# Performance work log

Hardware: AMD Instinct MI355X
Metric: run time of the kernel (lower is better)

The kernel has to match this reference:

```python
import jax, jax.numpy as jnp
import numpy as np

HID = 1024

def setup_inputs() -> dict:
    key = jax.random.key(0)
    k1, k2, k3, k4, k5 = jax.random.split(key, 5)
    B, S, H = 32, 2048, HID
    hidden = jax.random.normal(k1, (B, H), dtype=jnp.float32)
    encoder_outputs = jax.random.normal(k2, (B, S, 2 * H), dtype=jnp.float32)
    # nn.Linear(3H, H): weight (H, 3H), bias (H); nn.Linear(H, 1, bias=False): weight (1, H)
    lim_a = 1.0 / np.sqrt(3 * H)
    attn_w = jax.random.uniform(k3, (H, 3 * H), minval=-lim_a, maxval=lim_a, dtype=jnp.float32)
    attn_b = jax.random.uniform(k4, (H,), minval=-lim_a, maxval=lim_a, dtype=jnp.float32)
    lim_v = 1.0 / np.sqrt(H)
    v_w = jax.random.uniform(k5, (H,), minval=-lim_v, maxval=lim_v, dtype=jnp.float32)
    return {"hidden": hidden, "encoder_outputs": encoder_outputs,
            "attn_w": attn_w, "attn_b": attn_b, "v_w": v_w}

def reference(hidden, encoder_outputs, attn_w, attn_b, v_w):
    H = hidden.shape[-1]
    # Split attn weight: columns [:H] act on the repeated hidden, [H:] on encoder_outputs.
    # Avoids materializing the (B, S, 3H) concat; math is identical.
    w_h = attn_w[:, :H]        # (H, H)
    w_e = attn_w[:, H:]        # (H, 2H)
    hid_proj = hidden @ w_h.T + attn_b            # (B, H)
    enc_proj = jnp.einsum('bse,he->bsh', encoder_outputs, w_e)  # (B, S, H)
    energy = jnp.tanh(hid_proj[:, None, :] + enc_proj)          # (B, S, H)
    scores = jnp.einsum('bsh,h->bs', energy, v_w)               # (B, S)
    attention_weights = jax.nn.softmax(scores, axis=1)          # (B, S)
    context = jnp.einsum('bs,bse->be', attention_weights, encoder_outputs)  # (B, 2H)
    return (context, attention_weights)
```

## Files before the change

### kernel.cpp

```cpp
#include <hip/hip_runtime.h>
#include <hip/hip_bf16.h>

#define AS1 __attribute__((address_space(1)))
#define AS3 __attribute__((address_space(3)))

typedef __attribute__((ext_vector_type(4))) float  f32x4;
typedef __attribute__((ext_vector_type(8))) __bf16 bf16x8;
typedef __attribute__((ext_vector_type(2))) __bf16 bf16x2;
typedef __attribute__((ext_vector_type(4))) unsigned int uint4_;

static __device__ __forceinline__ unsigned short f2bf_rne(float f) {
    unsigned int u = __builtin_bit_cast(unsigned int, f);
    u += 0x7fffu + ((u >> 16) & 1u);
    return (unsigned short)(u >> 16);
}

static __device__ __forceinline__ unsigned int pack2(float a, float b) {
#if __has_builtin(__builtin_amdgcn_cvt_pk_bf16_f32)
    bf16x2 r = __builtin_amdgcn_cvt_pk_bf16_f32(a, b);
    return __builtin_bit_cast(unsigned int, r);
#else
    return (unsigned int)f2bf_rne(a) | ((unsigned int)f2bf_rne(b) << 16);
#endif
}

__global__ __launch_bounds__(256) void convwe_kernel(
    const float* __restrict__ attn_w, unsigned short* __restrict__ Bw)
{
    const int idx = (blockIdx.x * 256 + threadIdx.x) * 8;
    const int h = idx >> 11;
    const int e = idx & 2047;
    const float* src = attn_w + h * 3072 + 1024 + e;
    f32x4 v0 = *(const f32x4*)src;
    f32x4 v1 = *(const f32x4*)(src + 4);
    uint4_ o;
    o.x = pack2(v0.x, v0.y); o.y = pack2(v0.z, v0.w);
    o.z = pack2(v1.x, v1.y); o.w = pack2(v1.z, v1.w);
    *(uint4_*)(Bw + idx) = o;
}

__global__ __launch_bounds__(256) void hidproj_kernel(
    const float* __restrict__ hidden, const float* __restrict__ attn_w,
    const float* __restrict__ attn_b, float* __restrict__ hp)
{
    __shared__ float wrow[1024];
    const int h = blockIdx.x;
    const int t = threadIdx.x;
#pragma unroll
    for (int i = 0; i < 4; ++i) wrow[t + i * 256] = attn_w[h * 3072 + t + i * 256];
    __syncthreads();
    const int wave = t >> 6, lane = t & 63;
    const float bias = attn_b[h];
    for (int b = wave; b < 32; b += 4) {
        float s = 0.f;
#pragma unroll
        for (int j = 0; j < 16; ++j)
            s = fmaf(hidden[b * 1024 + lane + j * 64], wrow[lane + j * 64], s);
#pragma unroll
        for (int off = 1; off < 64; off <<= 1) s += __shfl_xor(s, off);
        if (lane == 0) hp[b * 1024 + h] = s + bias;
    }
}

__global__ __launch_bounds__(256) void gemm_score_kernel(
    const float* __restrict__ A,
    const unsigned short* __restrict__ Bw,
    const float* __restrict__ hp,
    const float* __restrict__ vw,
    float* __restrict__ scores)
{
    __shared__ unsigned short As[128 * 32];
    __shared__ unsigned short Bs[128 * 32];

    const int id    = blockIdx.x;
    const int group = id >> 6;
    const int lid   = id & 63;
    const int mt    = group * 8 + (lid & 7);
    const int nt    = lid >> 3;
    const long tile_m = (long)mt * 128;
    const int  tile_n = nt * 128;

    const int t    = threadIdx.x;
    const int wave = t >> 6;
    const int lane = t & 63;
    const int quad = lane >> 4;
    const int l15  = lane & 15;

    const int arow = t >> 2;
    const int akc  = (t & 3) * 8;
    const float* aptr0 = A + (tile_m + arow) * 2048 + akc;
    const float* aptr1 = aptr0 + 64 * 2048;
    unsigned short* ad0 = &As[t * 8];
    unsigned short* ad1 = &As[(256 + t) * 8];

    const int bc0 = wave * 128 + lane;
    const int bc1 = bc0 + 64;
    const unsigned short* bptr0 = Bw + (tile_n + (bc0 >> 2)) * 2048 + (bc0 & 3) * 8;
    const unsigned short* bptr1 = Bw + (tile_n + (bc1 >> 2)) * 2048 + (bc1 & 3) * 8;
    unsigned short* bd0 = &Bs[(wave * 2 + 0) * 512];
    unsigned short* bd1 = &Bs[(wave * 2 + 1) * 512];

    const int wm = (wave >> 1) * 64;
    const int wn = (wave & 1) * 64;

    int aoff[4], boff[4];
#pragma unroll
    for (int i = 0; i < 4; ++i) {
        aoff[i] = (wm + i * 16 + l15) * 32 + quad * 8;
        boff[i] = (wn + i * 16 + l15) * 32 + quad * 8;
    }

    f32x4 acc[4][4];
#pragma unroll
    for (int i = 0; i < 4; ++i)
#pragma unroll
        for (int j = 0; j < 4; ++j) acc[i][j] = (f32x4){0.f, 0.f, 0.f, 0.f};

    f32x4 av0 = *(const f32x4*)aptr0;
    f32x4 av1 = *(const f32x4*)(aptr0 + 4);
    f32x4 av2 = *(const f32x4*)aptr1;
    f32x4 av3 = *(const f32x4*)(aptr1 + 4);

    for (int kt = 0; kt < 64; ++kt) {
        __syncthreads();
        __builtin_amdgcn_global_load_lds((const AS1 void*)bptr0, (AS3 void*)bd0, 16, 0, 0);
        __builtin_amdgcn_global_load_lds((const AS1 void*)bptr1, (AS3 void*)bd1, 16, 0, 0);
        bptr0 += 32; bptr1 += 32;

        uint4_ w0, w1;
        w0.x = pack2(av0.x, av0.y); w0.y = pack2(av0.z, av0.w);
        w0.z = pack2(av1.x, av1.y); w0.w = pack2(av1.z, av1.w);
        w1.x = pack2(av2.x, av2.y); w1.y = pack2(av2.z, av2.w);
        w1.z = pack2(av3.x, av3.y); w1.w = pack2(av3.z, av3.w);
        *(uint4_*)ad0 = w0;
        *(uint4_*)ad1 = w1;

        if (kt < 63) {
            aptr0 += 32; aptr1 += 32;
            av0 = *(const f32x4*)aptr0;
            av1 = *(const f32x4*)(aptr0 + 4);
            av2 = *(const f32x4*)aptr1;
            av3 = *(const f32x4*)(aptr1 + 4);
        }
        __syncthreads();

        bf16x8 af[4], bfr[4];
#pragma unroll
        for (int i = 0; i < 4; ++i) af[i]  = *(const bf16x8*)(&As[aoff[i]]);
#pragma unroll
        for (int i = 0; i < 4; ++i) bfr[i] = *(const bf16x8*)(&Bs[boff[i]]);
#pragma unroll
        for (int mi = 0; mi < 4; ++mi)
#pragma unroll
            for (int ni = 0; ni < 4; ++ni)
                acc[mi][ni] = __builtin_amdgcn_mfma_f32_16x16x32_bf16(
                    af[mi], bfr[ni], acc[mi][ni], 0, 0, 0);
    }

    const int bidx = mt >> 4;
    float vwv[4], hpv[4];
#pragma unroll
    for (int ni = 0; ni < 4; ++ni) {
        const int n = tile_n + wn + ni * 16 + l15;
        vwv[ni] = vw[n];
        hpv[ni] = hp[bidx * 1024 + n];
    }
#pragma unroll
    for (int mi = 0; mi < 4; ++mi) {
#pragma unroll
        for (int r = 0; r < 4; ++r) {
            float s = 0.f;
#pragma unroll
            for (int ni = 0; ni < 4; ++ni) {
                float x = hpv[ni] + acc[mi][ni][r];
                x = fminf(fmaxf(x, -12.f), 12.f);
                const float e  = __expf(x + x);
                const float th = (e - 1.f) * __builtin_amdgcn_rcpf(e + 1.f);
                s = fmaf(vwv[ni], th, s);
            }
            s += __shfl_xor(s, 1);
            s += __shfl_xor(s, 2);
            s += __shfl_xor(s, 4);
            s += __shfl_xor(s, 8);
            if (l15 == 0)
                atomicAdd(&scores[tile_m + wm + mi * 16 + quad * 4 + r], s);
        }
    }
}

__global__ __launch_bounds__(256) void softmax_kernel(float* __restrict__ sc)
{
    __shared__ float red[8];
    const int b = blockIdx.x, t = threadIdx.x;
    const int wave = t >> 6, lane = t & 63;
    float* p = sc + b * 2048;
    float v[8];
#pragma unroll
    for (int i = 0; i < 8; ++i) v[i] = p[t + i * 256];
    float m = v[0];
#pragma unroll
    for (int i = 1; i < 8; ++i) m = fmaxf(m, v[i]);
#pragma unroll
    for (int off = 1; off < 64; off <<= 1) m = fmaxf(m, __shfl_xor(m, off));
    if (lane == 0) red[wave] = m;
    __syncthreads();
    m = fmaxf(fmaxf(red[0], red[1]), fmaxf(red[2], red[3]));
    float s = 0.f;
#pragma unroll
    for (int i = 0; i < 8; ++i) { v[i] = __expf(v[i] - m); s += v[i]; }
#pragma unroll
    for (int off = 1; off < 64; off <<= 1) s += __shfl_xor(s, off);
    if (lane == 0) red[4 + wave] = s;
    __syncthreads();
    s = red[4] + red[5] + red[6] + red[7];
    const float inv = 1.0f / s;
#pragma unroll
    for (int i = 0; i < 8; ++i) p[t + i * 256] = v[i] * inv;
}

__global__ __launch_bounds__(256) void context_kernel(
    const float* __restrict__ enc, const float* __restrict__ attn,
    float* __restrict__ ctx)
{
    const int b  = blockIdx.x >> 5;
    const int sc = blockIdx.x & 31;
    const int t  = threadIdx.x;
    const float* ep = enc + ((long)(b * 2048 + sc * 64)) * 2048 + t * 8;
    const float* ap = attn + b * 2048 + sc * 64;
    f32x4 a0 = (f32x4){0.f, 0.f, 0.f, 0.f};
    f32x4 a1 = (f32x4){0.f, 0.f, 0.f, 0.f};
#pragma unroll 4
    for (int s = 0; s < 64; ++s) {
        const float w = ap[s];
        f32x4 v0 = *(const f32x4*)ep;
        f32x4 v1 = *(const f32x4*)(ep + 4);
        a0 += w * v0;
        a1 += w * v1;
        ep += 2048;
    }
    float* cp = ctx + b * 2048 + t * 8;
    atomicAdd(&cp[0], a0.x); atomicAdd(&cp[1], a0.y);
    atomicAdd(&cp[2], a0.z); atomicAdd(&cp[3], a0.w);
    atomicAdd(&cp[4], a1.x); atomicAdd(&cp[5], a1.y);
    atomicAdd(&cp[6], a1.z); atomicAdd(&cp[7], a1.w);
}

extern "C" void kernel_launch(void* const* d_in, const int* in_sizes, int n_in,
                              void* d_out, int out_size, void* d_ws, size_t ws_size,
                              hipStream_t stream)
{
    const float* hidden = (const float*)d_in[0];
    const float* enc    = (const float*)d_in[1];
    const float* attn_w = (const float*)d_in[2];
    const float* attn_b = (const float*)d_in[3];
    const float* vw     = (const float*)d_in[4];
    float* out = (float*)d_out;

    unsigned short* Bw = (unsigned short*)d_ws;
    float* hp = (float*)((char*)d_ws + (size_t)1024 * 2048 * 2);

    float* ctx  = out;
    float* attn = out + 65536;

    hipMemsetAsync(d_out, 0, (size_t)out_size * 4, stream);
    convwe_kernel <<<1024, 256, 0, stream>>>(attn_w, Bw);
    hidproj_kernel<<<1024, 256, 0, stream>>>(hidden, attn_w, attn_b, hp);
    gemm_score_kernel<<<4096, 256, 0, stream>>>(enc, Bw, hp, vw, attn);
    softmax_kernel<<<32, 256, 0, stream>>>(attn);
    context_kernel<<<1024, 256, 0, stream>>>(enc, attn, ctx);
}
```

Measured before the change: 1.205 ms.

## Pre-convert encoder outputs to bf16 and split context into partial sums plus reduce

Adds a pass that converts the full encoder_outputs tensor to bf16 in workspace. The GEMM can then load both A and B tiles with direct global-to-LDS loads, so the per-iteration fp32 load and pack of A goes away. The context reduction also changes from per-element global atomics to per-chunk partial sums followed by a reduce kernel. Both paths are chosen only when the workspace is large enough. The conversion adds a 512MB read and a 256MB write, which may cost more than the GEMM saves.

```diff
diff --git a/kernel.cpp b/kernel.cpp
--- a/kernel.cpp
+++ b/kernel.cpp
@@ -39,6 +39,18 @@
     *(uint4_*)(Bw + idx) = o;
 }
 
+__global__ __launch_bounds__(256) void convenc_kernel(
+    const float* __restrict__ enc, unsigned short* __restrict__ dst)
+{
+    const size_t idx = ((size_t)blockIdx.x * 256 + threadIdx.x) * 8;
+    f32x4 v0 = *(const f32x4*)(enc + idx);
+    f32x4 v1 = *(const f32x4*)(enc + idx + 4);
+    uint4_ o;
+    o.x = pack2(v0.x, v0.y); o.y = pack2(v0.z, v0.w);
+    o.z = pack2(v1.x, v1.y); o.w = pack2(v1.z, v1.w);
+    *(uint4_*)(dst + idx) = o;
+}
+
 __global__ __launch_bounds__(256) void hidproj_kernel(
     const float* __restrict__ hidden, const float* __restrict__ attn_w,
     const float* __restrict__ attn_b, float* __restrict__ hp)
@@ -62,8 +74,8 @@
     }
 }
 
-__global__ __launch_bounds__(256) void gemm_score_kernel(
-    const float* __restrict__ A,
+__global__ __launch_bounds__(256) void gemm_score_bf16_kernel(
+    const unsigned short* __restrict__ Abf,
     const unsigned short* __restrict__ Bw,
     const float* __restrict__ hp,
     const float* __restrict__ vw,
@@ -86,19 +98,16 @@
     const int quad = lane >> 4;
     const int l15  = lane & 15;
 
-    const int arow = t >> 2;
-    const int akc  = (t & 3) * 8;
-    const float* aptr0 = A + (tile_m + arow) * 2048 + akc;
-    const float* aptr1 = aptr0 + 64 * 2048;
-    unsigned short* ad0 = &As[t * 8];
-    unsigned short* ad1 = &As[(256 + t) * 8];
-
-    const int bc0 = wave * 128 + lane;
-    const int bc1 = bc0 + 64;
-    const unsigned short* bptr0 = Bw + (tile_n + (bc0 >> 2)) * 2048 + (bc0 & 3) * 8;
-    const unsigned short* bptr1 = Bw + (tile_n + (bc1 >> 2)) * 2048 + (bc1 & 3) * 8;
-    unsigned short* bd0 = &Bs[(wave * 2 + 0) * 512];
-    unsigned short* bd1 = &Bs[(wave * 2 + 1) * 512];
+    const int ca = wave * 64 + lane;
+    const int cb = (4 + wave) * 64 + lane;
+    const unsigned short* apg0 = Abf + (tile_m + (ca >> 2)) * 2048 + (ca & 3) * 8;
+    const unsigned short* apg1 = Abf + (tile_m + (cb >> 2)) * 2048 + (cb & 3) * 8;
+    const unsigned short* bpg0 = Bw + (size_t)(tile_n + (ca >> 2)) * 2048 + (ca & 3) * 8;
+    const unsigned short* bpg1 = Bw + (size_t)(tile_n + (cb >> 2)) * 2048 + (cb & 3) * 8;
+    unsigned short* ald0 = &As[wave * 512];
+    unsigned short* ald1 = &As[(4 + wave) * 512];
+    unsigned short* bld0 = &Bs[wave * 512];
+    unsigned short* bld1 = &Bs[(4 + wave) * 512];
 
     const int wm = (wave >> 1) * 64;
     const int wn = (wave & 1) * 64;
@@ -116,32 +125,13 @@
 #pragma unroll
         for (int j = 0; j < 4; ++j) acc[i][j] = (f32x4){0.f, 0.f, 0.f, 0.f};
 
-    f32x4 av0 = *(const f32x4*)aptr0;
-    f32x4 av1 = *(const f32x4*)(aptr0 + 4);
-    f32x4 av2 = *(const f32x4*)aptr1;
-    f32x4 av3 = *(const f32x4*)(aptr1 + 4);
-
     for (int kt = 0; kt < 64; ++kt) {
         __syncthreads();
-        __builtin_amdgcn_global_load_lds((const AS1 void*)bptr0, (AS3 void*)bd0, 16, 0, 0);
-        __builtin_amdgcn_global_load_lds((const AS1 void*)bptr1, (AS3 void*)bd1, 16, 0, 0);
-        bptr0 += 32; bptr1 += 32;
-
-        uint4_ w0, w1;
-        w0.x = pack2(av0.x, av0.y); w0.y = pack2(av0.z, av0.w);
-        w0.z = pack2(av1.x, av1.y); w0.w = pack2(av1.z, av1.w);
-        w1.x = pack2(av2.x, av2.y); w1.y = pack2(av2.z, av2.w);
-        w1.z = pack2(av3.x, av3.y); w1.w = pack2(av3.z, av3.w);
-        *(uint4_*)ad0 = w0;
-        *(uint4_*)ad1 = w1;
-
-        if (kt < 63) {
-            aptr0 += 32; aptr1 += 32;
-            av0 = *(const f32x4*)aptr0;
-            av1 = *(const f32x4*)(aptr0 + 4);
-            av2 = *(const f32x4*)aptr1;
-            av3 = *(const f32x4*)(aptr1 + 4);
-        }
+        __builtin_amdgcn_global_load_lds((const AS1 void*)apg0, (AS3 void*)ald0, 16, 0, 0);
+        __builtin_amdgcn_global_load_lds((const AS1 void*)apg1, (AS3 void*)ald1, 16, 0, 0);
+        __builtin_amdgcn_global_load_lds((const AS1 void*)bpg0, (AS3 void*)bld0, 16, 0, 0);
+        __builtin_amdgcn_global_load_lds((const AS1 void*)bpg1, (AS3 void*)bld1, 16, 0, 0);
+        apg0 += 32; apg1 += 32; bpg0 += 32; bpg1 += 32;
         __syncthreads();
 
         bf16x8 af[4], bfr[4];
@@ -188,6 +178,112 @@
     }
 }
 
+__global__ __launch_bounds__(256) void gemm_score_kernel(
+    const float* __restrict__ A, const unsigned short* __restrict__ Bw,
+    const float* __restrict__ hp, const float* __restrict__ vw,
+    float* __restrict__ scores)
+{
+    __shared__ unsigned short As[128 * 32];
+    __shared__ unsigned short Bs[128 * 32];
+    const int id    = blockIdx.x;
+    const int group = id >> 6;
+    const int lid   = id & 63;
+    const int mt    = group * 8 + (lid & 7);
+    const int nt    = lid >> 3;
+    const long tile_m = (long)mt * 128;
+    const int  tile_n = nt * 128;
+    const int t = threadIdx.x, wave = t >> 6, lane = t & 63;
+    const int quad = lane >> 4, l15 = lane & 15;
+    const int arow = t >> 2, akc = (t & 3) * 8;
+    const float* aptr0 = A + (tile_m + arow) * 2048 + akc;
+    const float* aptr1 = aptr0 + 64 * 2048;
+    unsigned short* ad0 = &As[t * 8];
+    unsigned short* ad1 = &As[(256 + t) * 8];
+    const int bc0 = wave * 128 + lane;
+    const int bc1 = bc0 + 64;
+    const unsigned short* bptr0 = Bw + (tile_n + (bc0 >> 2)) * 2048 + (bc0 & 3) * 8;
+    const unsigned short* bptr1 = Bw + (tile_n + (bc1 >> 2)) * 2048 + (bc1 & 3) * 8;
+    unsigned short* bd0 = &Bs[(wave * 2 + 0) * 512];
+    unsigned short* bd1 = &Bs[(wave * 2 + 1) * 512];
+    const int wm = (wave >> 1) * 64, wn = (wave & 1) * 64;
+    int aoff[4], boff[4];
+#pragma unroll
+    for (int i = 0; i < 4; ++i) {
+        aoff[i] = (wm + i * 16 + l15) * 32 + quad * 8;
+        boff[i] = (wn + i * 16 + l15) * 32 + quad * 8;
+    }
+    f32x4 acc[4][4];
+#pragma unroll
+    for (int i = 0; i < 4; ++i)
+#pragma unroll
+        for (int j = 0; j < 4; ++j) acc[i][j] = (f32x4){0.f, 0.f, 0.f, 0.f};
+    f32x4 av0 = *(const f32x4*)aptr0;
+    f32x4 av1 = *(const f32x4*)(aptr0 + 4);
+    f32x4 av2 = *(const f32x4*)aptr1;
+    f32x4 av3 = *(const f32x4*)(aptr1 + 4);
+    for (int kt = 0; kt < 64; ++kt) {
+        __syncthreads();
+        __builtin_amdgcn_global_load_lds((const AS1 void*)bptr0, (AS3 void*)bd0, 16, 0, 0);
+        __builtin_amdgcn_global_load_lds((const AS1 void*)bptr1, (AS3 void*)bd1, 16, 0, 0);
+        bptr0 += 32; bptr1 += 32;
+        uint4_ w0, w1;
+        w0.x = pack2(av0.x, av0.y); w0.y = pack2(av0.z, av0.w);
+        w0.z = pack2(av1.x, av1.y); w0.w = pack2(av1.z, av1.w);
+        w1.x = pack2(av2.x, av2.y); w1.y = pack2(av2.z, av2.w);
+        w1.z = pack2(av3.x, av3.y); w1.w = pack2(av3.z, av3.w);
+        *(uint4_*)ad0 = w0;
+        *(uint4_*)ad1 = w1;
+        if (kt < 63) {
+            aptr0 += 32; aptr1 += 32;
+            av0 = *(const f32x4*)aptr0;
+            av1 = *(const f32x4*)(aptr0 + 4);
+            av2 = *(const f32x4*)aptr1;
+            av3 = *(const f32x4*)(aptr1 + 4);
+        }
+        __syncthreads();
+        bf16x8 af[4], bfr[4];
+#pragma unroll
+        for (int i = 0; i < 4; ++i) af[i]  = *(const bf16x8*)(&As[aoff[i]]);
+#pragma unroll
+        for (int i = 0; i < 4; ++i) bfr[i] = *(const bf16x8*)(&Bs[boff[i]]);
+#pragma unroll
+        for (int mi = 0; mi < 4; ++mi)
+#pragma unroll
+            for (int ni = 0; ni < 4; ++ni)
+                acc[mi][ni] = __builtin_amdgcn_mfma_f32_16x16x32_bf16(
+                    af[mi], bfr[ni], acc[mi][ni], 0, 0, 0);
+    }
+    const int bidx = mt >> 4;
+    float vwv[4], hpv[4];
+#pragma unroll
+    for (int ni = 0; ni < 4; ++ni) {
+        const int n = tile_n + wn + ni * 16 + l15;
+        vwv[ni] = vw[n];
+        hpv[ni] = hp[bidx * 1024 + n];
+    }
+#pragma unroll
+    for (int mi = 0; mi < 4; ++mi) {
+#pragma unroll
+        for (int r = 0; r < 4; ++r) {
+            float s = 0.f;
+#pragma unroll
+            for (int ni = 0; ni < 4; ++ni) {
+                float x = hpv[ni] + acc[mi][ni][r];
+                x = fminf(fmaxf(x, -12.f), 12.f);
+                const float e  = __expf(x + x);
+                const float th = (e - 1.f) * __builtin_amdgcn_rcpf(e + 1.f);
+                s = fmaf(vwv[ni], th, s);
+            }
+            s += __shfl_xor(s, 1);
+            s += __shfl_xor(s, 2);
+            s += __shfl_xor(s, 4);
+            s += __shfl_xor(s, 8);
+            if (l15 == 0)
+                atomicAdd(&scores[tile_m + wm + mi * 16 + quad * 4 + r], s);
+        }
+    }
+}
+
 __global__ __launch_bounds__(256) void softmax_kernel(float* __restrict__ sc)
 {
     __shared__ float red[8];
@@ -216,6 +312,43 @@
     const float inv = 1.0f / s;
 #pragma unroll
     for (int i = 0; i < 8; ++i) p[t + i * 256] = v[i] * inv;
+}
+
+__global__ __launch_bounds__(256) void context_part_kernel(
+    const float* __restrict__ enc, const float* __restrict__ attn,
+    float* __restrict__ part)
+{
+    const int b  = blockIdx.x >> 4;
+    const int sc = blockIdx.x & 15;
+    const int t  = threadIdx.x;
+    const float* ep = enc + ((size_t)(b * 2048 + sc * 128)) * 2048 + t * 8;
+    const float* ap = attn + b * 2048 + sc * 128;
+    f32x4 a0 = (f32x4){0.f, 0.f, 0.f, 0.f};
+    f32x4 a1 = (f32x4){0.f, 0.f, 0.f, 0.f};
+#pragma unroll 4
+    for (int s = 0; s < 128; ++s) {
+        const float w = ap[s];
+        f32x4 v0 = *(const f32x4*)ep;
+        f32x4 v1 = *(const f32x4*)(ep + 4);
+        a0 += w * v0;
+        a1 += w * v1;
+        ep += 2048;
+    }
+    float* pp = part + ((size_t)(b * 16 + sc)) * 2048 + t * 8;
+    *(f32x4*)pp = a0;
+    *(f32x4*)(pp + 4) = a1;
+}
+
+__global__ __launch_bounds__(256) void context_reduce_kernel(
+    const float* __restrict__ part, float* __restrict__ ctx)
+{
+    const int idx = blockIdx.x * 256 + threadIdx.x;
+    const int b = idx >> 11, e = idx & 2047;
+    const float* pp = part + ((size_t)b * 16) * 2048 + e;
+    float s = 0.f;
+#pragma unroll
+    for (int i = 0; i < 16; ++i) s += pp[i * 2048];
+    ctx[idx] = s;
 }
 
 __global__ __launch_bounds__(256) void context_kernel(
@@ -256,8 +389,17 @@
     const float* vw     = (const float*)d_in[4];
     float* out = (float*)d_out;
 
-    unsigned short* Bw = (unsigned short*)d_ws;
-    float* hp = (float*)((char*)d_ws + (size_t)1024 * 2048 * 2);
+    const size_t off_Bw   = 0;
+    const size_t off_hp   = (size_t)1024 * 2048 * 2;
+    const size_t off_part = off_hp + (size_t)32 * 1024 * 4;
+    const size_t off_enc  = off_part + (size_t)512 * 2048 * 4;
+    const size_t need_part = off_enc;
+    const size_t need_full = off_enc + (size_t)65536 * 2048 * 2;
+
+    unsigned short* Bw   = (unsigned short*)((char*)d_ws + off_Bw);
+    float*          hp   = (float*)((char*)d_ws + off_hp);
+    float*          part = (float*)((char*)d_ws + off_part);
+    unsigned short* encbf= (unsigned short*)((char*)d_ws + off_enc);
 
     float* ctx  = out;
     float* attn = out + 65536;
@@ -265,7 +407,20 @@
     hipMemsetAsync(d_out, 0, (size_t)out_size * 4, stream);
     convwe_kernel <<<1024, 256, 0, stream>>>(attn_w, Bw);
     hidproj_kernel<<<1024, 256, 0, stream>>>(hidden, attn_w, attn_b, hp);
-    gemm_score_kernel<<<4096, 256, 0, stream>>>(enc, Bw, hp, vw, attn);
+
+    if (ws_size >= need_full) {
+        convenc_kernel<<<65536, 256, 0, stream>>>(enc, encbf);
+        gemm_score_bf16_kernel<<<4096, 256, 0, stream>>>(encbf, Bw, hp, vw, attn);
+    } else {
+        gemm_score_kernel<<<4096, 256, 0, stream>>>(enc, Bw, hp, vw, attn);
+    }
+
     softmax_kernel<<<32, 256, 0, stream>>>(attn);
-    context_kernel<<<1024, 256, 0, stream>>>(enc, attn, ctx);
-}
+
+    if (ws_size >= need_part) {
+        context_part_kernel  <<<512, 256, 0, stream>>>(enc, attn, part);
+        context_reduce_kernel<<<256, 256, 0, stream>>>(part, ctx);
+    } else {
+        context_kernel<<<1024, 256, 0, stream>>>(enc, attn, ctx);
+    }
+}
```

After: 1.164 ms. 3.4% less time.
